# Optimization experiments

Hardware: AMD Instinct MI355X
Metric: run time of the kernel (lower is better)

## Reference

```python
import jax, jax.numpy as jnp
import numpy as np

L, C, K, V, G, T, NC, CIN = 9, 256, 3, 25, 9, 128, 60, 3


def _ln(x, w, b, axes, eps=1e-5):
    # LayerNorm over (channels, joints) per time step, affine params broadcast over time
    m = x.mean(axes, keepdims=True)
    v = x.var(axes, keepdims=True)
    return (x - m) * jax.lax.rsqrt(v + eps) * w + b


def setup_inputs() -> dict:
    key = jax.random.key(0)
    ks = jax.random.split(key, 8)
    s = 0.02  # weight init scale
    return {
        "x": jax.random.normal(ks[0], (1, CIN, T, V), jnp.float32),
        "A": jax.random.uniform(ks[1], (K, V, V), jnp.float32),
        "ln_in_w": jnp.ones((CIN, V), jnp.float32),
        "ln_in_b": jnp.zeros((CIN, V), jnp.float32),
        "W_in": jax.random.normal(ks[2], (C, CIN), jnp.float32) * s,
        "b_in": jnp.zeros((C,), jnp.float32),
        "Wg": jax.random.normal(ks[3], (L, K * C, C), jnp.float32) * s,
        "bg": jnp.zeros((L, K * C), jnp.float32),
        "ln1_w": jnp.ones((L, C, V), jnp.float32),
        "ln1_b": jnp.zeros((L, C, V), jnp.float32),
        "Wt": jax.random.normal(ks[4], (L, C, C, G), jnp.float32) * s,
        "bt": jnp.zeros((L, C), jnp.float32),
        "ln2_w": jnp.ones((L, C, V), jnp.float32),
        "ln2_b": jnp.zeros((L, C, V), jnp.float32),
        "imp": jnp.ones((L, K, V, V), jnp.float32),
        "W_out": jax.random.normal(ks[5], (NC, C), jnp.float32) * s,
        "b_out": jnp.zeros((NC,), jnp.float32),
    }


def reference(x, A, ln_in_w, ln_in_b, W_in, b_in, Wg, bg, ln1_w, ln1_b,
              Wt, bt, ln2_w, ln2_b, imp, W_out, b_out):
    ghalf = G // 2
    Al = A[None] * imp                      # (L, K, V, V) edge-importance weighted adjacency
    xs = x[0].transpose(1, 0, 2)            # (T, CIN, V): stream frames
    fifo0 = jnp.zeros((L, C, G, V), x.dtype)

    def step(carry, xt):
        fifo, fifo_res = carry
        # input LayerNorm + 1x1 conv (fcn_in)
        h = _ln(xt, ln_in_w, ln_in_b, (0, 1))
        h = jnp.einsum('oc,cv->ov', W_in, h) + b_in[:, None]   # (C, V)
        new_f, new_fr = [], []
        for l in range(L):
            res = h                                             # identity residual (in==out, stride==1)
            # graph conv: 1x1 conv -> (K, C, V), einsum with partitioned adjacency
            y = (jnp.einsum('oc,cv->ov', Wg[l], h) + bg[l][:, None]).reshape(K, C, V)
            z = jnp.einsum('kcv,kvw->cw', y, Al[l])             # (C, V)
            # FIFO shift: newest frame at time index 0
            f = jnp.concatenate([z[:, None, :], fifo[l, :, :-1]], axis=1)      # (C, G, V)
            fr = jnp.concatenate([res[:, None, :], fifo_res[l, :, :-1]], axis=1)
            # tcn: LN -> ReLU -> temporal conv (G,1) -> LN
            a = jax.nn.relu(_ln(f, ln1_w[l][:, None, :], ln1_b[l][:, None, :], (0, 2)))
            t = jnp.einsum('ocg,cgv->ov', Wt[l], a) + bt[l][:, None]           # (C, V)
            t = _ln(t, ln2_w[l], ln2_b[l], (0, 1))
            # residual from center of residual FIFO, then ReLU
            h = jax.nn.relu(t + fr[:, ghalf])
            new_f.append(f)
            new_fr.append(fr)
        pooled = h.mean(axis=1)                                 # avg_pool2d over (T=1, V)
        logits = W_out @ pooled + b_out                         # (NC,)
        return (jnp.stack(new_f), jnp.stack(new_fr)), logits

    _, out = jax.lax.scan(step, (fifo0, fifo0), xs)
    return out  # (T, NC): per-frame class logits
```

## Files before the change

### kernel.cpp

```cpp
#include <hip/hip_runtime.h>

#define TT  128
#define CC  256
#define VV  25
#define KK  3
#define GG  9
#define LL  9
#define NCC 60
#define CINN 3
#define TV    (TT*VV)
#define N4    4096
#define KDIM2 (CC*GG)
#define UR    ((TT+8)*32)
#define YSTR  104
#define HSTR  264
#define FSTR  33

typedef __attribute__((ext_vector_type(8))) short bf16x8;
typedef __attribute__((ext_vector_type(4))) float f32x4;
typedef unsigned short us16;

__device__ __forceinline__ us16 f2bf(float f) {
    union { float f; unsigned u; } a; a.f = f;
    unsigned r = a.u + 0x7fff + ((a.u >> 16) & 1);
    return (us16)(r >> 16);
}
__device__ __forceinline__ bf16x8 ld8(const us16* p) { return *(const bf16x8*)p; }


#define PN1 (LL*KK*CC*CC)
#define PN2 (LL*CC*CC*GG)
#define PN3 (LL*KK*32*32)
#define PN4 (LL*CC*32)
#define PTOT (PN1+PN2+PN3+PN4)

__global__ void k_prep(const float* __restrict__ Wg, const float* __restrict__ Wt,
                       const float* __restrict__ A, const float* __restrict__ imp,
                       const float* __restrict__ bg,
                       us16* __restrict__ Wgb, us16* __restrict__ Wt2b,
                       us16* __restrict__ AlTb, float* __restrict__ bgAl) {
    int i = blockIdx.x * 256 + threadIdx.x;
    if (i < PN1) {
        Wgb[i] = f2bf(Wg[i]);
    } else if (i < PN1 + PN2) {
        int j = i - PN1;
        int kk = j % (CC*GG);
        int o  = (j / (CC*GG)) % CC;
        int l  = j / (CC*CC*GG);
        int g = kk >> 8, c = kk & 255;
        Wt2b[j] = f2bf(Wt[((size_t)(l*CC + o)*CC + c)*GG + g]);
    } else if (i < PN1 + PN2 + PN3) {
        int j = i - PN1 - PN2;
        int v = j & 31, w = (j >> 5) & 31;
        int lk = j >> 10, k = lk % KK, l = lk / KK;
        float val = 0.f;
        if (v < VV && w < VV)
            val = A[(k*VV+v)*VV + w] * imp[((size_t)(l*KK+k)*VV+v)*VV + w];
        AlTb[j] = f2bf(val);
    } else if (i < PTOT) {
        int j = i - PN1 - PN2 - PN3;
        int w = j & 31, c = (j >> 5) & 255, l = j >> 13;
        float s = 0.f;
        if (w < VV) {
            for (int k = 0; k < KK; k++) {
                float col = 0.f;
                for (int v = 0; v < VV; v++)
                    col += A[(k*VV+v)*VV + w] * imp[((size_t)(l*KK+k)*VV+v)*VV + w];
                s += bg[l*KK*CC + k*CC + c] * col;
            }
        }
        bgAl[j] = s;
    }
}


__device__ __forceinline__ void blk_reduce2(float& s, float& q, float* red) {
    #pragma unroll
    for (int off = 32; off; off >>= 1) {
        s += __shfl_down(s, off);
        q += __shfl_down(q, off);
    }
    int lane = threadIdx.x & 63, w = threadIdx.x >> 6;
    if (lane == 0) { red[w] = s; red[4+w] = q; }
    __syncthreads();
    s = red[0]+red[1]+red[2]+red[3];
    q = red[4]+red[5]+red[6]+red[7];
}


template<int FIRST>
__global__ __launch_bounds__(256) void k_gcn(
    const float* __restrict__ x, const float* __restrict__ lniw,
    const float* __restrict__ lnib, const float* __restrict__ Win,
    const float* __restrict__ bin,
    const float* __restrict__ TC, const float* __restrict__ btv,
    const float* __restrict__ ln2w, const float* __restrict__ ln2b,
    const float* __restrict__ HresidT,
    const us16* __restrict__ Wgb,
    const us16* __restrict__ AlTb, const float* __restrict__ bgAl,
    const float* __restrict__ lnw, const float* __restrict__ lnb,
    float* __restrict__ HT, us16* __restrict__ Ut2) {

    const int t = blockIdx.x, tid = threadIdx.x;
    if (t >= TT) {
        int tp = t - TT, c = tid;
        #pragma unroll
        for (int w = 0; w < 32; w++) {
            float u = (w < VV) ? fmaxf(lnb[c*VV + w], 0.f) : 0.f;
            Ut2[(size_t)(tp*32 + w)*CC + c] = f2bf(u);
        }
        return;
    }
    __shared__ __align__(16) us16 pool[CC*YSTR];
    __shared__ __align__(16) us16 sH[32*HSTR];
    __shared__ float red[8];
    __shared__ float sx[80];
    __shared__ float sh[80];
    const int wave = tid >> 6, lane = tid & 63, quad = lane >> 4, l16 = lane & 15;

    if (FIRST) {
        if (tid < CINN*VV)
            sx[tid] = x[(size_t)(tid/VV)*TV + t*VV + (tid%VV)];
        __syncthreads();
        float s = 0.f, q = 0.f;
        for (int i = 0; i < CINN*VV; i++) { float v = sx[i]; s += v; q += v*v; }
        float m  = s * (1.f/75.f);
        float var = q * (1.f/75.f) - m*m;
        float rs = rsqrtf(var + 1e-5f);
        if (tid < CINN*VV)
            sh[tid] = (sx[tid]-m)*rs*lniw[tid] + lnib[tid];
        __syncthreads();
        int c = tid;
        float w0 = Win[c*3+0], w1 = Win[c*3+1], w2 = Win[c*3+2], bb = bin[c];
        #pragma unroll
        for (int v = 0; v < VV; v++) {
            float acc = bb + w0*sh[v] + w1*sh[VV+v] + w2*sh[2*VV+v];
            HT[(size_t)(t*32 + v)*CC + c] = acc;
            sH[v*HSTR + c] = f2bf(acc);
        }
        #pragma unroll
        for (int v = VV; v < 32; v++)
            sH[v*HSTR + c] = 0;
        __syncthreads();
    } else {
        float* sF = (float*)pool;
        #pragma unroll
        for (int j = 0; j < 8; j++) {
            int cs = j*32 + (tid >> 3);
            int v4 = (tid & 7) * 4;
            float4 xv = *(const float4*)(TC + (size_t)cs*N4 + t*32 + v4);
            sF[cs*FSTR + v4+0] = xv.x; sF[cs*FSTR + v4+1] = xv.y;
            sF[cs*FSTR + v4+2] = xv.z; sF[cs*FSTR + v4+3] = xv.w;
        }
        __syncthreads();
        int c = tid;
        float btc = btv[c];
        float vals[VV];
        float s = 0.f, q = 0.f;
        #pragma unroll
        for (int v = 0; v < VV; v++) {
            float xv = sF[c*FSTR + v] + btc;
            vals[v] = xv; s += xv; q += xv*xv;
        }
        blk_reduce2(s, q, red);
        float m = s * (1.f/6400.f);
        float var = q * (1.f/6400.f) - m*m;
        float rs = rsqrtf(var + 1e-5f);
        #pragma unroll
        for (int v = 0; v < VV; v++) {
            float res = (t >= 4) ? HresidT[(size_t)((t-4)*32 + v)*CC + c] : 0.f;
            float o = fmaxf((vals[v]-m)*rs*ln2w[c*VV+v] + ln2b[c*VV+v] + res, 0.f);
            HT[(size_t)(t*32 + v)*CC + c] = o;
            sH[v*HSTR + c] = f2bf(o);
        }
        #pragma unroll
        for (int v = VV; v < 32; v++)
            sH[v*HSTR + c] = 0;
        __syncthreads();
    }

    us16* Yt = pool;
    bf16x8 bf[2][8];
    #pragma unroll
    for (int nt = 0; nt < 2; nt++)
        #pragma unroll
        for (int s = 0; s < 8; s++)
            bf[nt][s] = *(const bf16x8*)(sH + (nt*16 + l16)*HSTR + s*32 + quad*8);
    f32x4 acc[12][2];
    #pragma unroll
    for (int mt = 0; mt < 12; mt++) { acc[mt][0] = (f32x4){}; acc[mt][1] = (f32x4){}; }
    #pragma unroll
    for (int mt = 0; mt < 12; mt++) {
        const us16* ap = Wgb + (size_t)(wave*192 + mt*16 + l16)*CC + quad*8;
        #pragma unroll
        for (int s = 0; s < 8; s++) {
            bf16x8 a = ld8(ap + s*32);
            acc[mt][0] = __builtin_amdgcn_mfma_f32_16x16x32_bf16(a, bf[0][s], acc[mt][0], 0,0,0);
            acc[mt][1] = __builtin_amdgcn_mfma_f32_16x16x32_bf16(a, bf[1][s], acc[mt][1], 0,0,0);
        }
    }
    __syncthreads();
    #pragma unroll
    for (int mt = 0; mt < 12; mt++)
        #pragma unroll
        for (int nt = 0; nt < 2; nt++)
            #pragma unroll
            for (int r = 0; r < 4; r++) {
                int m = wave*192 + mt*16 + quad*4 + r;
                Yt[(m & 255)*YSTR + (m >> 8)*32 + nt*16 + l16] = f2bf(acc[mt][nt][r]);
            }
    __syncthreads();

    bf16x8 al[2][3];
    #pragma unroll
    for (int nt = 0; nt < 2; nt++)
        #pragma unroll
        for (int s = 0; s < 3; s++)
            al[nt][s] = ld8(AlTb + (size_t)(s*32 + nt*16 + l16)*32 + quad*8);
    f32x4 z[4][2];
    #pragma unroll
    for (int mt = 0; mt < 4; mt++) { z[mt][0] = (f32x4){}; z[mt][1] = (f32x4){}; }
    #pragma unroll
    for (int mt = 0; mt < 4; mt++)
        #pragma unroll
        for (int s = 0; s < 3; s++) {
            bf16x8 a = *(const bf16x8*)(Yt + (wave*64 + mt*16 + l16)*YSTR + s*32 + quad*8);
            z[mt][0] = __builtin_amdgcn_mfma_f32_16x16x32_bf16(a, al[0][s], z[mt][0], 0,0,0);
            z[mt][1] = __builtin_amdgcn_mfma_f32_16x16x32_bf16(a, al[1][s], z[mt][1], 0,0,0);
        }

    float s_ = 0.f, q_ = 0.f;
    #pragma unroll
    for (int mt = 0; mt < 4; mt++)
        #pragma unroll
        for (int nt = 0; nt < 2; nt++)
            #pragma unroll
            for (int r = 0; r < 4; r++) {
                int c = wave*64 + mt*16 + quad*4 + r;
                int w = nt*16 + l16;
                float zb = z[mt][nt][r] + bgAl[c*32 + w];
                z[mt][nt][r] = zb;
                if (w < VV) { s_ += zb; q_ += zb*zb; }
            }
    blk_reduce2(s_, q_, red);
    float m = s_ * (1.f/6400.f);
    float var = q_ * (1.f/6400.f) - m*m;
    float rs = rsqrtf(var + 1e-5f);
    #pragma unroll
    for (int mt = 0; mt < 4; mt++)
        #pragma unroll
        for (int nt = 0; nt < 2; nt++) {
            int w = nt*16 + l16;
            if (w < VV) {
                int c0 = wave*64 + mt*16 + quad*4;
                ushort4 pk;
                float u0 = fmaxf((z[mt][nt][0]-m)*rs*lnw[(c0+0)*VV+w] + lnb[(c0+0)*VV+w], 0.f);
                float u1 = fmaxf((z[mt][nt][1]-m)*rs*lnw[(c0+1)*VV+w] + lnb[(c0+1)*VV+w], 0.f);
                float u2 = fmaxf((z[mt][nt][2]-m)*rs*lnw[(c0+2)*VV+w] + lnb[(c0+2)*VV+w], 0.f);
                float u3 = fmaxf((z[mt][nt][3]-m)*rs*lnw[(c0+3)*VV+w] + lnb[(c0+3)*VV+w], 0.f);
                pk.x = f2bf(u0); pk.y = f2bf(u1); pk.z = f2bf(u2); pk.w = f2bf(u3);
                *(ushort4*)(Ut2 + (size_t)((t+8)*32 + w)*CC + c0) = pk;
            }
        }
    #pragma unroll
    for (int r = VV; r < 32; r++)
        Ut2[(size_t)((t+8)*32 + r)*CC + tid] = 0;
}


__global__ __launch_bounds__(256) void k_gemm2(const us16* __restrict__ A,
                                               const us16* __restrict__ Ut2,
                                               float* __restrict__ TC) {
    const int tid = threadIdx.x;
    const int wave = tid >> 6, lane = tid & 63, quad = lane >> 4, l16 = lane & 15;
    const int m0w = blockIdx.y * 64 + (wave & 1) * 32;
    const int n0w = blockIdx.x * 64 + (wave >> 1) * 32;
    const us16* ap = A + (size_t)(m0w + l16) * KDIM2 + quad * 8;
    f32x4 acc00 = {}, acc01 = {}, acc10 = {}, acc11 = {};
    bf16x8 a0[2], a1[2], b0[2], b1[2];

    auto loadAB = [&](int k0, bf16x8& x0, bf16x8& x1, bf16x8& y0, bf16x8& y1) {
        x0 = ld8(ap + k0);
        x1 = ld8(ap + k0 + 16*KDIM2);
        int g = k0 >> 8;
        const us16* bp = Ut2 + (size_t)(n0w + (8-g)*32 + l16)*CC + (k0 & 255) + quad*8;
        y0 = ld8(bp);
        y1 = ld8(bp + 16*CC);
    };
    auto domfma = [&](bf16x8 x0, bf16x8 x1, bf16x8 y0, bf16x8 y1) {
        acc00 = __builtin_amdgcn_mfma_f32_16x16x32_bf16(x0, y0, acc00, 0,0,0);
        acc01 = __builtin_amdgcn_mfma_f32_16x16x32_bf16(x0, y1, acc01, 0,0,0);
        acc10 = __builtin_amdgcn_mfma_f32_16x16x32_bf16(x1, y0, acc10, 0,0,0);
        acc11 = __builtin_amdgcn_mfma_f32_16x16x32_bf16(x1, y1, acc11, 0,0,0);
    };

    loadAB(0,  a0[0], a1[0], b0[0], b1[0]);
    loadAB(32, a0[1], a1[1], b0[1], b1[1]);
    #pragma unroll 2
    for (int k0 = 64; k0 < KDIM2; k0 += 32) {
        int sl = (k0 >> 5) & 1;
        bf16x8 ta0 = a0[sl], ta1 = a1[sl], tb0 = b0[sl], tb1 = b1[sl];
        loadAB(k0, a0[sl], a1[sl], b0[sl], b1[sl]);
        domfma(ta0, ta1, tb0, tb1);
    }
    domfma(a0[0], a1[0], b0[0], b1[0]);
    domfma(a0[1], a1[1], b0[1], b1[1]);

    const int r0 = m0w + quad*4;
    const int col = n0w + l16;
    #pragma unroll
    for (int r = 0; r < 4; r++) {
        TC[(size_t)(r0 + r)*N4 + col]           = acc00[r];
        TC[(size_t)(r0 + r)*N4 + col + 16]      = acc01[r];
        TC[(size_t)(r0 + 16 + r)*N4 + col]      = acc10[r];
        TC[(size_t)(r0 + 16 + r)*N4 + col + 16] = acc11[r];
    }
}


__global__ __launch_bounds__(256) void k_fin(const float* __restrict__ TC,
                                             const float* __restrict__ HresidT,
                                             const float* __restrict__ btv,
                                             const float* __restrict__ lnw,
                                             const float* __restrict__ lnb,
                                             const float* __restrict__ Wout,
                                             const float* __restrict__ bout,
                                             float* __restrict__ out) {
    int t = blockIdx.x, tid = threadIdx.x;
    __shared__ float sF[CC*FSTR];
    __shared__ float red[8];
    __shared__ float sp[CC];
    #pragma unroll
    for (int j = 0; j < 8; j++) {
        int cs = j*32 + (tid >> 3);
        int v4 = (tid & 7) * 4;
        float4 xv = *(const float4*)(TC + (size_t)cs*N4 + t*32 + v4);
        sF[cs*FSTR + v4+0] = xv.x; sF[cs*FSTR + v4+1] = xv.y;
        sF[cs*FSTR + v4+2] = xv.z; sF[cs*FSTR + v4+3] = xv.w;
    }
    __syncthreads();
    int c = tid;
    float btc = btv[c];
    float vals[VV];
    float s = 0.f, q = 0.f;
    #pragma unroll
    for (int v = 0; v < VV; v++) {
        float xv = sF[c*FSTR + v] + btc;
        vals[v] = xv; s += xv; q += xv*xv;
    }
    blk_reduce2(s, q, red);
    float m = s * (1.f/6400.f);
    float var = q * (1.f/6400.f) - m*m;
    float rs = rsqrtf(var + 1e-5f);
    float pl = 0.f;
    #pragma unroll
    for (int v = 0; v < VV; v++) {
        float res = (t >= 4) ? HresidT[(size_t)((t-4)*32 + v)*CC + c] : 0.f;
        float o = fmaxf((vals[v]-m)*rs*lnw[c*VV+v] + lnb[c*VV+v] + res, 0.f);
        pl += o;
    }
    sp[c] = pl * (1.f/VV);
    __syncthreads();
    if (tid < NCC) {
        float a = bout[tid];
        for (int cc = 0; cc < CC; cc++) a = fmaf(Wout[tid*CC+cc], sp[cc], a);
        out[t*NCC + tid] = a;
    }
}


extern "C" void kernel_launch(void* const* d_in, const int* in_sizes, int n_in,
                              void* d_out, int out_size, void* d_ws, size_t ws_size,
                              hipStream_t stream) {
    const float* x    = (const float*)d_in[0];
    const float* A    = (const float*)d_in[1];
    const float* lniw = (const float*)d_in[2];
    const float* lnib = (const float*)d_in[3];
    const float* Win  = (const float*)d_in[4];
    const float* bin  = (const float*)d_in[5];
    const float* Wg   = (const float*)d_in[6];
    const float* bg   = (const float*)d_in[7];
    const float* ln1w = (const float*)d_in[8];
    const float* ln1b = (const float*)d_in[9];
    const float* Wt   = (const float*)d_in[10];
    const float* bt   = (const float*)d_in[11];
    const float* ln2w = (const float*)d_in[12];
    const float* ln2b = (const float*)d_in[13];
    const float* imp  = (const float*)d_in[14];
    const float* Wout = (const float*)d_in[15];
    const float* bout = (const float*)d_in[16];
    float* out = (float*)d_out;

    float* ws = (float*)d_ws;
    size_t off = 0;
    auto alloc = [&](size_t n) { float* p = ws + off; off += (n + 255) & ~(size_t)255; return p; };
    float* HT0  = alloc((size_t)TT*32*CC);
    float* HT1  = alloc((size_t)TT*32*CC);
    float* TC   = alloc((size_t)CC*N4);
    float* bgAl = alloc((size_t)LL*CC*32);
    us16* Wgb  = (us16*)alloc((size_t)LL*KK*CC*CC/2);
    us16* Wt2b = (us16*)alloc((size_t)LL*CC*KDIM2/2);
    us16* Ut2  = (us16*)alloc((size_t)UR*CC/2);
    us16* AlTb = (us16*)alloc((size_t)LL*KK*32*32/2);
    (void)ws_size; (void)in_sizes; (void)n_in; (void)out_size;

    k_prep<<<(PTOT + 255)/256, 256, 0, stream>>>(Wg, Wt, A, imp, bg,
                                                 Wgb, Wt2b, AlTb, bgAl);

    float* hPrev = HT0; float* hNext = HT1;
    for (int l = 0; l < LL; l++) {
        if (l == 0) {
            k_gcn<1><<<TT + 8, 256, 0, stream>>>(
                x, lniw, lnib, Win, bin,
                TC, bt, ln2w, ln2b, hPrev,
                Wgb, AlTb, bgAl, ln1w, ln1b,
                hPrev , Ut2);
        } else {
            k_gcn<0><<<TT + 8, 256, 0, stream>>>(
                x, lniw, lnib, Win, bin,
                TC, bt + (size_t)(l-1)*CC,
                ln2w + (size_t)(l-1)*CC*VV, ln2b + (size_t)(l-1)*CC*VV,
                hPrev ,
                Wgb + (size_t)l*KK*CC*CC,
                AlTb + (size_t)l*KK*32*32, bgAl + (size_t)l*CC*32,
                ln1w + (size_t)l*CC*VV, ln1b + (size_t)l*CC*VV,
                hNext , Ut2);
            float* tmp = hPrev; hPrev = hNext; hNext = tmp;
        }
        k_gemm2<<<dim3(64, 4), 256, 0, stream>>>(
            Wt2b + (size_t)l*CC*KDIM2, Ut2, TC);
    }
    k_fin<<<TT, 256, 0, stream>>>(TC, hPrev,
        bt + (size_t)(LL-1)*CC, ln2w + (size_t)(LL-1)*CC*VV, ln2b + (size_t)(LL-1)*CC*VV,
        Wout, bout, out);
}
```

Before: 785.8 us.

## Split temporal-conv GEMM along K into two partial buffers summed by consumers

The temporal-conv GEMM now runs with a third grid dimension that splits the K range (C*G) in half, so each block writes a partial result to its own buffer. The downstream gcn and final kernels read both partial buffers and add them while loading into shared memory. The aim is to double the block count from 256 to 512 to fill more of the GPU's compute units and shorten each block's serial K loop. The inner loop is also restructured into two explicit register buffers with a launch-bounds occupancy hint. In exchange it doubles the TC workspace and adds extra global write and read traffic for the partials.

```diff
diff --git a/kernel.cpp b/kernel.cpp
--- a/kernel.cpp
+++ b/kernel.cpp
@@ -11,6 +11,8 @@
 #define TV    (TT*VV)
 #define N4    4096
 #define KDIM2 (CC*GG)
+#define KS    2
+#define KCH   (KDIM2/KS)
 #define UR    ((TT+8)*32)
 #define YSTR  104
 #define HSTR  264
@@ -93,7 +95,7 @@
     const float* __restrict__ x, const float* __restrict__ lniw,
     const float* __restrict__ lnib, const float* __restrict__ Win,
     const float* __restrict__ bin,
-    const float* __restrict__ TC, const float* __restrict__ btv,
+    const float* __restrict__ TCp, const float* __restrict__ btv,
     const float* __restrict__ ln2w, const float* __restrict__ ln2b,
     const float* __restrict__ HresidT,
     const us16* __restrict__ Wgb,
@@ -148,9 +150,11 @@
         for (int j = 0; j < 8; j++) {
             int cs = j*32 + (tid >> 3);
             int v4 = (tid & 7) * 4;
-            float4 xv = *(const float4*)(TC + (size_t)cs*N4 + t*32 + v4);
-            sF[cs*FSTR + v4+0] = xv.x; sF[cs*FSTR + v4+1] = xv.y;
-            sF[cs*FSTR + v4+2] = xv.z; sF[cs*FSTR + v4+3] = xv.w;
+            size_t base = (size_t)cs*N4 + t*32 + v4;
+            float4 xv = *(const float4*)(TCp + base);
+            float4 yv = *(const float4*)(TCp + (size_t)CC*N4 + base);
+            sF[cs*FSTR + v4+0] = xv.x + yv.x; sF[cs*FSTR + v4+1] = xv.y + yv.y;
+            sF[cs*FSTR + v4+2] = xv.z + yv.z; sF[cs*FSTR + v4+3] = xv.w + yv.w;
         }
         __syncthreads();
         int c = tid;
@@ -268,43 +272,47 @@
 }
 
 
-__global__ __launch_bounds__(256) void k_gemm2(const us16* __restrict__ A,
-                                               const us16* __restrict__ Ut2,
-                                               float* __restrict__ TC) {
+__global__ __launch_bounds__(256, 2) void k_gemm2(const us16* __restrict__ A,
+                                                  const us16* __restrict__ Ut2,
+                                                  float* __restrict__ TCp) {
     const int tid = threadIdx.x;
     const int wave = tid >> 6, lane = tid & 63, quad = lane >> 4, l16 = lane & 15;
     const int m0w = blockIdx.y * 64 + (wave & 1) * 32;
     const int n0w = blockIdx.x * 64 + (wave >> 1) * 32;
+    const int kbeg = blockIdx.z * KCH;
+    float* TC = TCp + (size_t)blockIdx.z * CC * N4;
     const us16* ap = A + (size_t)(m0w + l16) * KDIM2 + quad * 8;
     f32x4 acc00 = {}, acc01 = {}, acc10 = {}, acc11 = {};
-    bf16x8 a0[2], a1[2], b0[2], b1[2];
-
-    auto loadAB = [&](int k0, bf16x8& x0, bf16x8& x1, bf16x8& y0, bf16x8& y1) {
-        x0 = ld8(ap + k0);
-        x1 = ld8(ap + k0 + 16*KDIM2);
+
+    bf16x8 xa0, xa1, xb0, xb1;
+    bf16x8 ya0, ya1, yb0, yb1;
+
+    auto ldc = [&](int k0, bf16x8& A0, bf16x8& A1, bf16x8& B0, bf16x8& B1) {
+        A0 = ld8(ap + k0);
+        A1 = ld8(ap + k0 + 16*KDIM2);
         int g = k0 >> 8;
         const us16* bp = Ut2 + (size_t)(n0w + (8-g)*32 + l16)*CC + (k0 & 255) + quad*8;
-        y0 = ld8(bp);
-        y1 = ld8(bp + 16*CC);
+        B0 = ld8(bp);
+        B1 = ld8(bp + 16*CC);
     };
-    auto domfma = [&](bf16x8 x0, bf16x8 x1, bf16x8 y0, bf16x8 y1) {
-        acc00 = __builtin_amdgcn_mfma_f32_16x16x32_bf16(x0, y0, acc00, 0,0,0);
-        acc01 = __builtin_amdgcn_mfma_f32_16x16x32_bf16(x0, y1, acc01, 0,0,0);
-        acc10 = __builtin_amdgcn_mfma_f32_16x16x32_bf16(x1, y0, acc10, 0,0,0);
-        acc11 = __builtin_amdgcn_mfma_f32_16x16x32_bf16(x1, y1, acc11, 0,0,0);
+    auto mf = [&](bf16x8 A0, bf16x8 A1, bf16x8 B0, bf16x8 B1) {
+        acc00 = __builtin_amdgcn_mfma_f32_16x16x32_bf16(A0, B0, acc00, 0,0,0);
+        acc01 = __builtin_amdgcn_mfma_f32_16x16x32_bf16(A0, B1, acc01, 0,0,0);
+        acc10 = __builtin_amdgcn_mfma_f32_16x16x32_bf16(A1, B0, acc10, 0,0,0);
+        acc11 = __builtin_amdgcn_mfma_f32_16x16x32_bf16(A1, B1, acc11, 0,0,0);
     };
 
-    loadAB(0,  a0[0], a1[0], b0[0], b1[0]);
-    loadAB(32, a0[1], a1[1], b0[1], b1[1]);
-    #pragma unroll 2
-    for (int k0 = 64; k0 < KDIM2; k0 += 32) {
-        int sl = (k0 >> 5) & 1;
-        bf16x8 ta0 = a0[sl], ta1 = a1[sl], tb0 = b0[sl], tb1 = b1[sl];
-        loadAB(k0, a0[sl], a1[sl], b0[sl], b1[sl]);
-        domfma(ta0, ta1, tb0, tb1);
-    }
-    domfma(a0[0], a1[0], b0[0], b1[0]);
-    domfma(a0[1], a1[1], b0[1], b1[1]);
+    ldc(kbeg,      xa0, xa1, xb0, xb1);
+    ldc(kbeg + 32, ya0, ya1, yb0, yb1);
+    #pragma unroll 4
+    for (int k0 = kbeg + 64; k0 < kbeg + KCH; k0 += 64) {
+        mf(xa0, xa1, xb0, xb1);
+        ldc(k0, xa0, xa1, xb0, xb1);
+        mf(ya0, ya1, yb0, yb1);
+        ldc(k0 + 32, ya0, ya1, yb0, yb1);
+    }
+    mf(xa0, xa1, xb0, xb1);
+    mf(ya0, ya1, yb0, yb1);
 
     const int r0 = m0w + quad*4;
     const int col = n0w + l16;
@@ -318,7 +326,7 @@
 }
 
 
-__global__ __launch_bounds__(256) void k_fin(const float* __restrict__ TC,
+__global__ __launch_bounds__(256) void k_fin(const float* __restrict__ TCp,
                                              const float* __restrict__ HresidT,
                                              const float* __restrict__ btv,
                                              const float* __restrict__ lnw,
@@ -334,9 +342,11 @@
     for (int j = 0; j < 8; j++) {
         int cs = j*32 + (tid >> 3);
         int v4 = (tid & 7) * 4;
-        float4 xv = *(const float4*)(TC + (size_t)cs*N4 + t*32 + v4);
-        sF[cs*FSTR + v4+0] = xv.x; sF[cs*FSTR + v4+1] = xv.y;
-        sF[cs*FSTR + v4+2] = xv.z; sF[cs*FSTR + v4+3] = xv.w;
+        size_t base = (size_t)cs*N4 + t*32 + v4;
+        float4 xv = *(const float4*)(TCp + base);
+        float4 yv = *(const float4*)(TCp + (size_t)CC*N4 + base);
+        sF[cs*FSTR + v4+0] = xv.x + yv.x; sF[cs*FSTR + v4+1] = xv.y + yv.y;
+        sF[cs*FSTR + v4+2] = xv.z + yv.z; sF[cs*FSTR + v4+3] = xv.w + yv.w;
     }
     __syncthreads();
     int c = tid;
@@ -396,7 +406,7 @@
     auto alloc = [&](size_t n) { float* p = ws + off; off += (n + 255) & ~(size_t)255; return p; };
     float* HT0  = alloc((size_t)TT*32*CC);
     float* HT1  = alloc((size_t)TT*32*CC);
-    float* TC   = alloc((size_t)CC*N4);
+    float* TCp  = alloc((size_t)KS*CC*N4);
     float* bgAl = alloc((size_t)LL*CC*32);
     us16* Wgb  = (us16*)alloc((size_t)LL*KK*CC*CC/2);
     us16* Wt2b = (us16*)alloc((size_t)LL*CC*KDIM2/2);
@@ -412,13 +422,13 @@
         if (l == 0) {
             k_gcn<1><<<TT + 8, 256, 0, stream>>>(
                 x, lniw, lnib, Win, bin,
-                TC, bt, ln2w, ln2b, hPrev,
+                TCp, bt, ln2w, ln2b, hPrev,
                 Wgb, AlTb, bgAl, ln1w, ln1b,
                 hPrev , Ut2);
         } else {
             k_gcn<0><<<TT + 8, 256, 0, stream>>>(
                 x, lniw, lnib, Win, bin,
-                TC, bt + (size_t)(l-1)*CC,
+                TCp, bt + (size_t)(l-1)*CC,
                 ln2w + (size_t)(l-1)*CC*VV, ln2b + (size_t)(l-1)*CC*VV,
                 hPrev ,
                 Wgb + (size_t)l*KK*CC*CC,
@@ -427,10 +437,10 @@
                 hNext , Ut2);
             float* tmp = hPrev; hPrev = hNext; hNext = tmp;
         }
-        k_gemm2<<<dim3(64, 4), 256, 0, stream>>>(
-            Wt2b + (size_t)l*CC*KDIM2, Ut2, TC);
-    }
-    k_fin<<<TT, 256, 0, stream>>>(TC, hPrev,
+        k_gemm2<<<dim3(64, 4, KS), 256, 0, stream>>>(
+            Wt2b + (size_t)l*CC*KDIM2, Ut2, TCp);
+    }
+    k_fin<<<TT, 256, 0, stream>>>(TCp, hPrev,
         bt + (size_t)(LL-1)*CC, ln2w + (size_t)(LL-1)*CC*VV, ln2b + (size_t)(LL-1)*CC*VV,
         Wout, bout, out);
 }
```

New measurement: 811.8 us. 1.03x slower.

## Store intermediates as bf16 transposed, remap gemm2 blocks across XCDs, deepen prefetch

Applied to the files above, without the earlier changes.

The temporal-conv GEMM now writes its output in bf16, transposed through shared memory into a (time*joint, channel) layout. This lets the next graph-conv kernel and the final kernel read it directly with coalesced per-channel loads instead of staging fp32 tiles through LDS. The residual activations HT are also stored in bf16, which halves that traffic. k_gemm2 uses a 1D grid with an XCD-aware tile mapping and a 4-deep register prefetch pipeline. The cost is extra bf16 rounding on the residual and intermediate paths, which may reduce accuracy.

```diff
diff --git a/kernel.cpp b/kernel.cpp
--- a/kernel.cpp
+++ b/kernel.cpp
@@ -14,7 +14,6 @@
 #define UR    ((TT+8)*32)
 #define YSTR  104
 #define HSTR  264
-#define FSTR  33
 
 typedef __attribute__((ext_vector_type(8))) short bf16x8;
 typedef __attribute__((ext_vector_type(4))) float f32x4;
@@ -24,6 +23,9 @@
     union { float f; unsigned u; } a; a.f = f;
     unsigned r = a.u + 0x7fff + ((a.u >> 16) & 1);
     return (us16)(r >> 16);
+}
+__device__ __forceinline__ float bf2f(us16 u) {
+    union { unsigned u; float f; } a; a.u = ((unsigned)u) << 16; return a.f;
 }
 __device__ __forceinline__ bf16x8 ld8(const us16* p) { return *(const bf16x8*)p; }
 
@@ -93,13 +95,13 @@
     const float* __restrict__ x, const float* __restrict__ lniw,
     const float* __restrict__ lnib, const float* __restrict__ Win,
     const float* __restrict__ bin,
-    const float* __restrict__ TC, const float* __restrict__ btv,
+    const us16* __restrict__ Tt, const float* __restrict__ btv,
     const float* __restrict__ ln2w, const float* __restrict__ ln2b,
-    const float* __restrict__ HresidT,
+    const us16* __restrict__ HresidTb,
     const us16* __restrict__ Wgb,
     const us16* __restrict__ AlTb, const float* __restrict__ bgAl,
     const float* __restrict__ lnw, const float* __restrict__ lnb,
-    float* __restrict__ HT, us16* __restrict__ Ut2) {
+    us16* __restrict__ HTb, us16* __restrict__ Ut2) {
 
     const int t = blockIdx.x, tid = threadIdx.x;
     if (t >= TT) {
@@ -111,7 +113,7 @@
         }
         return;
     }
-    __shared__ __align__(16) us16 pool[CC*YSTR];
+    __shared__ __align__(16) us16 Yt[CC*YSTR];
     __shared__ __align__(16) us16 sH[32*HSTR];
     __shared__ float red[8];
     __shared__ float sx[80];
@@ -135,31 +137,22 @@
         #pragma unroll
         for (int v = 0; v < VV; v++) {
             float acc = bb + w0*sh[v] + w1*sh[VV+v] + w2*sh[2*VV+v];
-            HT[(size_t)(t*32 + v)*CC + c] = acc;
-            sH[v*HSTR + c] = f2bf(acc);
+            us16 b = f2bf(acc);
+            HTb[(size_t)(t*32 + v)*CC + c] = b;
+            sH[v*HSTR + c] = b;
         }
         #pragma unroll
         for (int v = VV; v < 32; v++)
             sH[v*HSTR + c] = 0;
         __syncthreads();
     } else {
-        float* sF = (float*)pool;
-        #pragma unroll
-        for (int j = 0; j < 8; j++) {
-            int cs = j*32 + (tid >> 3);
-            int v4 = (tid & 7) * 4;
-            float4 xv = *(const float4*)(TC + (size_t)cs*N4 + t*32 + v4);
-            sF[cs*FSTR + v4+0] = xv.x; sF[cs*FSTR + v4+1] = xv.y;
-            sF[cs*FSTR + v4+2] = xv.z; sF[cs*FSTR + v4+3] = xv.w;
-        }
-        __syncthreads();
         int c = tid;
         float btc = btv[c];
         float vals[VV];
         float s = 0.f, q = 0.f;
         #pragma unroll
         for (int v = 0; v < VV; v++) {
-            float xv = sF[c*FSTR + v] + btc;
+            float xv = bf2f(Tt[(size_t)(t*32 + v)*CC + c]) + btc;
             vals[v] = xv; s += xv; q += xv*xv;
         }
         blk_reduce2(s, q, red);
@@ -168,10 +161,11 @@
         float rs = rsqrtf(var + 1e-5f);
         #pragma unroll
         for (int v = 0; v < VV; v++) {
-            float res = (t >= 4) ? HresidT[(size_t)((t-4)*32 + v)*CC + c] : 0.f;
+            float res = (t >= 4) ? bf2f(HresidTb[(size_t)((t-4)*32 + v)*CC + c]) : 0.f;
             float o = fmaxf((vals[v]-m)*rs*ln2w[c*VV+v] + ln2b[c*VV+v] + res, 0.f);
-            HT[(size_t)(t*32 + v)*CC + c] = o;
-            sH[v*HSTR + c] = f2bf(o);
+            us16 b = f2bf(o);
+            HTb[(size_t)(t*32 + v)*CC + c] = b;
+            sH[v*HSTR + c] = b;
         }
         #pragma unroll
         for (int v = VV; v < 32; v++)
@@ -179,7 +173,6 @@
         __syncthreads();
     }
 
-    us16* Yt = pool;
     bf16x8 bf[2][8];
     #pragma unroll
     for (int nt = 0; nt < 2; nt++)
@@ -199,7 +192,6 @@
             acc[mt][1] = __builtin_amdgcn_mfma_f32_16x16x32_bf16(a, bf[1][s], acc[mt][1], 0,0,0);
         }
     }
-    __syncthreads();
     #pragma unroll
     for (int mt = 0; mt < 12; mt++)
         #pragma unroll
@@ -270,56 +262,69 @@
 
 __global__ __launch_bounds__(256) void k_gemm2(const us16* __restrict__ A,
                                                const us16* __restrict__ Ut2,
-                                               float* __restrict__ TC) {
+                                               us16* __restrict__ Tt) {
+    __shared__ us16 TL[64*72];
     const int tid = threadIdx.x;
     const int wave = tid >> 6, lane = tid & 63, quad = lane >> 4, l16 = lane & 15;
-    const int m0w = blockIdx.y * 64 + (wave & 1) * 32;
-    const int n0w = blockIdx.x * 64 + (wave >> 1) * 32;
-    const us16* ap = A + (size_t)(m0w + l16) * KDIM2 + quad * 8;
+    const int bid = blockIdx.x;
+    const int xcd = bid & 7, grp = bid >> 3;
+    const int mt = (xcd >> 2)*2 + (grp & 1);
+    const int nt = (xcd & 3)*16 + (grp >> 1);
+    const int m0b = mt*64, n0b = nt*64;
+    const int m0w = m0b + (wave & 1)*32;
+    const int n0w = n0b + (wave >> 1)*32;
+    const us16* ap = A + (size_t)(m0w + l16)*KDIM2 + quad*8;
     f32x4 acc00 = {}, acc01 = {}, acc10 = {}, acc11 = {};
-    bf16x8 a0[2], a1[2], b0[2], b1[2];
-
-    auto loadAB = [&](int k0, bf16x8& x0, bf16x8& x1, bf16x8& y0, bf16x8& y1) {
-        x0 = ld8(ap + k0);
-        x1 = ld8(ap + k0 + 16*KDIM2);
-        int g = k0 >> 8;
-        const us16* bp = Ut2 + (size_t)(n0w + (8-g)*32 + l16)*CC + (k0 & 255) + quad*8;
-        y0 = ld8(bp);
-        y1 = ld8(bp + 16*CC);
-    };
-    auto domfma = [&](bf16x8 x0, bf16x8 x1, bf16x8 y0, bf16x8 y1) {
-        acc00 = __builtin_amdgcn_mfma_f32_16x16x32_bf16(x0, y0, acc00, 0,0,0);
-        acc01 = __builtin_amdgcn_mfma_f32_16x16x32_bf16(x0, y1, acc01, 0,0,0);
-        acc10 = __builtin_amdgcn_mfma_f32_16x16x32_bf16(x1, y0, acc10, 0,0,0);
-        acc11 = __builtin_amdgcn_mfma_f32_16x16x32_bf16(x1, y1, acc11, 0,0,0);
-    };
-
-    loadAB(0,  a0[0], a1[0], b0[0], b1[0]);
-    loadAB(32, a0[1], a1[1], b0[1], b1[1]);
-    #pragma unroll 2
-    for (int k0 = 64; k0 < KDIM2; k0 += 32) {
-        int sl = (k0 >> 5) & 1;
-        bf16x8 ta0 = a0[sl], ta1 = a1[sl], tb0 = b0[sl], tb1 = b1[sl];
-        loadAB(k0, a0[sl], a1[sl], b0[sl], b1[sl]);
-        domfma(ta0, ta1, tb0, tb1);
-    }
-    domfma(a0[0], a1[0], b0[0], b1[0]);
-    domfma(a0[1], a1[1], b0[1], b1[1]);
-
-    const int r0 = m0w + quad*4;
-    const int col = n0w + l16;
+    bf16x8 aA0,aA1,bA0,bA1, aB0,aB1,bB0,bB1, aC0,aC1,bC0,bC1, aD0,aD1,bD0,bD1;
+
+#define GLD(S, it) { \
+    int k0 = (it)*32; \
+    a##S##0 = ld8(ap + k0); \
+    a##S##1 = ld8(ap + k0 + 16*KDIM2); \
+    int g = k0 >> 8; \
+    const us16* bp = Ut2 + (size_t)(n0w + (8-g)*32 + l16)*CC + (k0 & 255) + quad*8; \
+    b##S##0 = ld8(bp); \
+    b##S##1 = ld8(bp + 16*CC); }
+#define GMF(S) { \
+    acc00 = __builtin_amdgcn_mfma_f32_16x16x32_bf16(a##S##0, b##S##0, acc00,0,0,0); \
+    acc01 = __builtin_amdgcn_mfma_f32_16x16x32_bf16(a##S##0, b##S##1, acc01,0,0,0); \
+    acc10 = __builtin_amdgcn_mfma_f32_16x16x32_bf16(a##S##1, b##S##0, acc10,0,0,0); \
+    acc11 = __builtin_amdgcn_mfma_f32_16x16x32_bf16(a##S##1, b##S##1, acc11,0,0,0); }
+
+    GLD(A, 0); GLD(B, 1); GLD(C, 2); GLD(D, 3);
+    #pragma unroll 1
+    for (int it = 4; it <= KDIM2/32 - 4; it += 4) {
+        GMF(A); GLD(A, it);
+        GMF(B); GLD(B, it+1);
+        GMF(C); GLD(C, it+2);
+        GMF(D); GLD(D, it+3);
+    }
+    GMF(A); GMF(B); GMF(C); GMF(D);
+#undef GLD
+#undef GMF
+
     #pragma unroll
     for (int r = 0; r < 4; r++) {
-        TC[(size_t)(r0 + r)*N4 + col]           = acc00[r];
-        TC[(size_t)(r0 + r)*N4 + col + 16]      = acc01[r];
-        TC[(size_t)(r0 + 16 + r)*N4 + col]      = acc10[r];
-        TC[(size_t)(r0 + 16 + r)*N4 + col + 16] = acc11[r];
-    }
-}
-
-
-__global__ __launch_bounds__(256) void k_fin(const float* __restrict__ TC,
-                                             const float* __restrict__ HresidT,
+        int mlo = (wave & 1)*32 + quad*4 + r;
+        int nlo = (wave >> 1)*32 + l16;
+        TL[nlo*72 + mlo]           = f2bf(acc00[r]);
+        TL[(nlo+16)*72 + mlo]      = f2bf(acc01[r]);
+        TL[nlo*72 + mlo + 16]      = f2bf(acc10[r]);
+        TL[(nlo+16)*72 + mlo + 16] = f2bf(acc11[r]);
+    }
+    __syncthreads();
+    #pragma unroll
+    for (int u = 0; u < 2; u++) {
+        int q2 = tid + u*256;
+        int row = q2 >> 3, ch = q2 & 7;
+        *(bf16x8*)(Tt + (size_t)(n0b + row)*CC + m0b + ch*8) =
+            *(const bf16x8*)(TL + row*72 + ch*8);
+    }
+}
+
+
+__global__ __launch_bounds__(256) void k_fin(const us16* __restrict__ Tt,
+                                             const us16* __restrict__ HresidTb,
                                              const float* __restrict__ btv,
                                              const float* __restrict__ lnw,
                                              const float* __restrict__ lnb,
@@ -327,25 +332,15 @@
                                              const float* __restrict__ bout,
                                              float* __restrict__ out) {
     int t = blockIdx.x, tid = threadIdx.x;
-    __shared__ float sF[CC*FSTR];
     __shared__ float red[8];
     __shared__ float sp[CC];
-    #pragma unroll
-    for (int j = 0; j < 8; j++) {
-        int cs = j*32 + (tid >> 3);
-        int v4 = (tid & 7) * 4;
-        float4 xv = *(const float4*)(TC + (size_t)cs*N4 + t*32 + v4);
-        sF[cs*FSTR + v4+0] = xv.x; sF[cs*FSTR + v4+1] = xv.y;
-        sF[cs*FSTR + v4+2] = xv.z; sF[cs*FSTR + v4+3] = xv.w;
-    }
-    __syncthreads();
     int c = tid;
     float btc = btv[c];
     float vals[VV];
     float s = 0.f, q = 0.f;
     #pragma unroll
     for (int v = 0; v < VV; v++) {
-        float xv = sF[c*FSTR + v] + btc;
+        float xv = bf2f(Tt[(size_t)(t*32 + v)*CC + c]) + btc;
         vals[v] = xv; s += xv; q += xv*xv;
     }
     blk_reduce2(s, q, red);
@@ -355,7 +350,7 @@
     float pl = 0.f;
     #pragma unroll
     for (int v = 0; v < VV; v++) {
-        float res = (t >= 4) ? HresidT[(size_t)((t-4)*32 + v)*CC + c] : 0.f;
+        float res = (t >= 4) ? bf2f(HresidTb[(size_t)((t-4)*32 + v)*CC + c]) : 0.f;
         float o = fmaxf((vals[v]-m)*rs*lnw[c*VV+v] + lnb[c*VV+v] + res, 0.f);
         pl += o;
     }
@@ -394,10 +389,10 @@
     float* ws = (float*)d_ws;
     size_t off = 0;
     auto alloc = [&](size_t n) { float* p = ws + off; off += (n + 255) & ~(size_t)255; return p; };
-    float* HT0  = alloc((size_t)TT*32*CC);
-    float* HT1  = alloc((size_t)TT*32*CC);
-    float* TC   = alloc((size_t)CC*N4);
     float* bgAl = alloc((size_t)LL*CC*32);
+    us16* HTb0 = (us16*)alloc((size_t)TT*32*CC/2);
+    us16* HTb1 = (us16*)alloc((size_t)TT*32*CC/2);
+    us16* Tt   = (us16*)alloc((size_t)N4*CC/2);
     us16* Wgb  = (us16*)alloc((size_t)LL*KK*CC*CC/2);
     us16* Wt2b = (us16*)alloc((size_t)LL*CC*KDIM2/2);
     us16* Ut2  = (us16*)alloc((size_t)UR*CC/2);
@@ -407,30 +402,30 @@
     k_prep<<<(PTOT + 255)/256, 256, 0, stream>>>(Wg, Wt, A, imp, bg,
                                                  Wgb, Wt2b, AlTb, bgAl);
 
-    float* hPrev = HT0; float* hNext = HT1;
+    us16* hPrev = HTb0; us16* hNext = HTb1;
     for (int l = 0; l < LL; l++) {
         if (l == 0) {
             k_gcn<1><<<TT + 8, 256, 0, stream>>>(
                 x, lniw, lnib, Win, bin,
-                TC, bt, ln2w, ln2b, hPrev,
+                Tt, bt, ln2w, ln2b, hPrev,
                 Wgb, AlTb, bgAl, ln1w, ln1b,
                 hPrev , Ut2);
         } else {
             k_gcn<0><<<TT + 8, 256, 0, stream>>>(
                 x, lniw, lnib, Win, bin,
-                TC, bt + (size_t)(l-1)*CC,
+                Tt, bt + (size_t)(l-1)*CC,
                 ln2w + (size_t)(l-1)*CC*VV, ln2b + (size_t)(l-1)*CC*VV,
                 hPrev ,
                 Wgb + (size_t)l*KK*CC*CC,
                 AlTb + (size_t)l*KK*32*32, bgAl + (size_t)l*CC*32,
                 ln1w + (size_t)l*CC*VV, ln1b + (size_t)l*CC*VV,
                 hNext , Ut2);
-            float* tmp = hPrev; hPrev = hNext; hNext = tmp;
-        }
-        k_gemm2<<<dim3(64, 4), 256, 0, stream>>>(
-            Wt2b + (size_t)l*CC*KDIM2, Ut2, TC);
-    }
-    k_fin<<<TT, 256, 0, stream>>>(TC, hPrev,
+            us16* tmp = hPrev; hPrev = hNext; hNext = tmp;
+        }
+        k_gemm2<<<256, 256, 0, stream>>>(
+            Wt2b + (size_t)l*CC*KDIM2, Ut2, Tt);
+    }
+    k_fin<<<TT, 256, 0, stream>>>(Tt, hPrev,
         bt + (size_t)(LL-1)*CC, ln2w + (size_t)(LL-1)*CC*VV, ln2b + (size_t)(LL-1)*CC*VV,
         Wout, bout, out);
 }
```

Result: slower. 805.5 us (+2.5%).
